# Performance work log

Hardware: AMD Instinct MI355X
Metric: run time of the kernel (lower is better)

Reference implementation:

```python
import jax, jax.numpy as jnp
import numpy as np

M, K, N, G = 64, 4096, 11008, 128  # tokens, infeatures, outfeatures, group_size
NUM_GROUPS = K // G  # 32


def _fp8_round_trip(w):
    # Simulate FP8 E4M3 storage of the quantized weight codes.
    return w.astype(jnp.float8_e4m3fn).astype(jnp.float32)


def setup_inputs() -> dict:
    key = jax.random.key(0)
    k1, k2, k3, k4 = jax.random.split(key, 4)
    x = jax.random.normal(k1, (M, K), dtype=jnp.float32)
    # FP8-representable weight codes (post round-trip, stored as f32 values)
    weight = _fp8_round_trip(jax.random.normal(k2, (N, K), dtype=jnp.float32) * 2.0)
    # Per-(out_feature, group) dequant scales, strictly positive
    weight_scale = jax.random.uniform(k3, (N, NUM_GROUPS), dtype=jnp.float32,
                                      minval=0.005, maxval=0.02)
    bias = jax.random.normal(k4, (N,), dtype=jnp.float32)
    return {"x": x, "weight": weight, "weight_scale": weight_scale, "bias": bias}


def reference(x, weight, weight_scale, bias):
    # Dequantize: each group of `G` consecutive in-features of an output row
    # shares one scale -> w_deq[o, i] = weight[o, i] * scale[o, i // G]
    n, k = weight.shape
    g = k // weight_scale.shape[1]
    w_deq = (weight.reshape(n, -1, g) * weight_scale[:, :, None]).reshape(n, k)
    # Fused dequant-matmul: out[m, o] = sum_i x[m, i] * w_deq[o, i] + bias[o]
    out = jnp.einsum("mk,nk->mn", x, w_deq) + bias
    return out
```

## Files before the change

kernel.cpp:

```cpp
#include <hip/hip_runtime.h>


#define Md 64
#define Kd 4096
#define Nd 11008
#define NGROUPS 32
#define BN 64
#define BK 64
#define KSPLIT 8
#define KCHUNK (Kd / KSPLIT)
#define NITER (KCHUNK / BK)
#define NGRP (KCHUNK / 128)
#define XLD (BK + 8)

typedef __attribute__((ext_vector_type(8))) __bf16 bf16x8;
typedef __attribute__((ext_vector_type(4))) float f32x4;

__global__ __launch_bounds__(256, 4)
void qlinear_pass1(const float* __restrict__ x,
                   const float* __restrict__ w,
                   const float* __restrict__ scale,
                   float* __restrict__ ws)
{
    const int tid  = threadIdx.x;
    const int wv   = tid >> 6;
    const int lane = tid & 63;
    const int quad = lane >> 4;
    const int ln   = lane & 15;

    const int n0 = blockIdx.x * BN;
    const int ky = blockIdx.y;
    const int k0 = ky * KCHUNK;

    const int nrow = n0 + wv * 16 + ln;
    const float* wp = w + (size_t)nrow * Kd + k0 + quad * 8;

    const int xrow = tid >> 2;
    const int xc0  = (tid & 3) * 16;
    const float* xp = x + (size_t)xrow * Kd + k0 + xc0;

    __shared__ __bf16 lds_x[Md * XLD];

    float4 sc4 = *(const float4*)(scale + (size_t)nrow * NGROUPS + ky * NGRP);
    const float sc[4] = {sc4.x, sc4.y, sc4.z, sc4.w};

    f32x4 acc[4];
    #pragma unroll
    for (int t = 0; t < 4; ++t) acc[t] = (f32x4){0.f, 0.f, 0.f, 0.f};

    float4 wreg[2][4], xreg[2][4];
    #pragma unroll
    for (int j = 0; j < 4; ++j)
        xreg[0][j] = *(const float4*)(xp + j * 4);
    wreg[0][0] = *(const float4*)(wp + 0);
    wreg[0][1] = *(const float4*)(wp + 4);
    wreg[0][2] = *(const float4*)(wp + 32);
    wreg[0][3] = *(const float4*)(wp + 36);

    #pragma unroll
    for (int g = 0; g < NGRP; ++g) {
        f32x4 pg[4];
        #pragma unroll
        for (int t = 0; t < 4; ++t) pg[t] = (f32x4){0.f, 0.f, 0.f, 0.f};

        #pragma unroll
        for (int sub = 0; sub < 2; ++sub) {
            const int i   = g * 2 + sub;
            const int buf = i & 1;

            #pragma unroll
            for (int j = 0; j < 2; ++j) {
                float4 a = xreg[buf][2 * j], b = xreg[buf][2 * j + 1];
                bf16x8 v = {(__bf16)a.x, (__bf16)a.y, (__bf16)a.z, (__bf16)a.w,
                            (__bf16)b.x, (__bf16)b.y, (__bf16)b.z, (__bf16)b.w};
                *(bf16x8*)&lds_x[xrow * XLD + xc0 + j * 8] = v;
            }
            __syncthreads();

            if (i + 1 < NITER) {
                const int nb = buf ^ 1;
                #pragma unroll
                for (int j = 0; j < 4; ++j)
                    xreg[nb][j] = *(const float4*)(xp + (i + 1) * BK + j * 4);
                wreg[nb][0] = *(const float4*)(wp + (i + 1) * BK + 0);
                wreg[nb][1] = *(const float4*)(wp + (i + 1) * BK + 4);
                wreg[nb][2] = *(const float4*)(wp + (i + 1) * BK + 32);
                wreg[nb][3] = *(const float4*)(wp + (i + 1) * BK + 36);
            }

            #pragma unroll
            for (int ks = 0; ks < 2; ++ks) {
                float4 wa = wreg[buf][2 * ks], wb = wreg[buf][2 * ks + 1];
                bf16x8 wf = {(__bf16)wa.x, (__bf16)wa.y, (__bf16)wa.z, (__bf16)wa.w,
                             (__bf16)wb.x, (__bf16)wb.y, (__bf16)wb.z, (__bf16)wb.w};
                #pragma unroll
                for (int t = 0; t < 4; ++t) {
                    bf16x8 xf = *(const bf16x8*)
                        &lds_x[(t * 16 + ln) * XLD + ks * 32 + quad * 8];
                    pg[t] = __builtin_amdgcn_mfma_f32_16x16x32_bf16(xf, wf, pg[t],
                                                                    0, 0, 0);
                }
            }
            __syncthreads();
        }

        const float s = sc[g];
        #pragma unroll
        for (int t = 0; t < 4; ++t)
            #pragma unroll
            for (int r = 0; r < 4; ++r)
                acc[t][r] += s * pg[t][r];
    }

    float* op = ws + ((size_t)ky * Md) * Nd + n0 + wv * 16 + ln;
    #pragma unroll
    for (int t = 0; t < 4; ++t)
        #pragma unroll
        for (int r = 0; r < 4; ++r)
            op[(size_t)(t * 16 + quad * 4 + r) * Nd] = acc[t][r];
}

__global__ __launch_bounds__(256)
void qlinear_reduce(const float* __restrict__ ws,
                    const float* __restrict__ bias,
                    float* __restrict__ out)
{
    const int idx = blockIdx.x * 256 + threadIdx.x;
    if (idx >= Md * Nd) return;
    const int n = idx % Nd;
    float v = bias[n];
    #pragma unroll
    for (int ky = 0; ky < KSPLIT; ++ky)
        v += ws[(size_t)ky * Md * Nd + idx];
    out[idx] = v;
}

extern "C" void kernel_launch(void* const* d_in, const int* in_sizes, int n_in,
                              void* d_out, int out_size, void* d_ws, size_t ws_size,
                              hipStream_t stream) {
    const float* x     = (const float*)d_in[0];
    const float* w     = (const float*)d_in[1];
    const float* scale = (const float*)d_in[2];
    const float* bias  = (const float*)d_in[3];
    float* out = (float*)d_out;
    float* ws  = (float*)d_ws;

    dim3 grid1(Nd / BN, KSPLIT);
    qlinear_pass1<<<grid1, 256, 0, stream>>>(x, w, scale, ws);

    const int total = Md * Nd;
    qlinear_reduce<<<(total + 255) / 256, 256, 0, stream>>>(ws, bias, out);
}
```

Baseline: 275.4 us.

## Pre-convert activations to MFMA-fragment bf16 layout and drop LDS staging

Adds an xprep kernel that converts x to bf16 once, laid out in MFMA fragment order. The main kernel can then load activation fragments straight from global memory (L2-resident) instead of each block converting x, staging it in LDS and synchronising twice per iteration. It also removes the explicit register double-buffering of weight loads and vectorises the split-K reduce to float4. The trade-offs are an extra kernel launch and reliance on the compiler and cache to hide load latency without the manual prefetch.

After: 279.6 us. About the same (+1.5%).

```diff
diff --git a/kernel.cpp b/kernel.cpp
--- a/kernel.cpp
+++ b/kernel.cpp
@@ -6,19 +6,34 @@
 #define Nd 11008
 #define NGROUPS 32
 #define BN 64
-#define BK 64
 #define KSPLIT 8
 #define KCHUNK (Kd / KSPLIT)
-#define NITER (KCHUNK / BK)
 #define NGRP (KCHUNK / 128)
-#define XLD (BK + 8)
+#define KBC (KCHUNK / 32)
 
 typedef __attribute__((ext_vector_type(8))) __bf16 bf16x8;
 typedef __attribute__((ext_vector_type(4))) float f32x4;
 
+
+__global__ __launch_bounds__(256)
+void xprep(const float* __restrict__ x, __bf16* __restrict__ xf)
+{
+    const int tid  = blockIdx.x * 256 + threadIdx.x;
+    const int lane = tid & 63;
+    const int t    = (tid >> 6) & 3;
+    const int kb   = tid >> 8;
+    const int row  = t * 16 + (lane & 15);
+    const int col  = kb * 32 + (lane >> 4) * 8;
+    const float4 a = *(const float4*)(x + (size_t)row * Kd + col);
+    const float4 b = *(const float4*)(x + (size_t)row * Kd + col + 4);
+    bf16x8 v = {(__bf16)a.x, (__bf16)a.y, (__bf16)a.z, (__bf16)a.w,
+                (__bf16)b.x, (__bf16)b.y, (__bf16)b.z, (__bf16)b.w};
+    *(bf16x8*)(xf + (size_t)tid * 8) = v;
+}
+
 __global__ __launch_bounds__(256, 4)
-void qlinear_pass1(const float* __restrict__ x,
-                   const float* __restrict__ w,
+void qlinear_pass1(const float* __restrict__ w,
+                   const __bf16* __restrict__ xf,
                    const float* __restrict__ scale,
                    float* __restrict__ ws)
 {
@@ -35,11 +50,7 @@
     const int nrow = n0 + wv * 16 + ln;
     const float* wp = w + (size_t)nrow * Kd + k0 + quad * 8;
 
-    const int xrow = tid >> 2;
-    const int xc0  = (tid & 3) * 16;
-    const float* xp = x + (size_t)xrow * Kd + k0 + xc0;
-
-    __shared__ __bf16 lds_x[Md * XLD];
+    const __bf16* xp = xf + (size_t)ky * KBC * 4 * 512 + lane * 8;
 
     float4 sc4 = *(const float4*)(scale + (size_t)nrow * NGROUPS + ky * NGRP);
     const float sc[4] = {sc4.x, sc4.y, sc4.z, sc4.w};
@@ -48,15 +59,6 @@
     #pragma unroll
     for (int t = 0; t < 4; ++t) acc[t] = (f32x4){0.f, 0.f, 0.f, 0.f};
 
-    float4 wreg[2][4], xreg[2][4];
-    #pragma unroll
-    for (int j = 0; j < 4; ++j)
-        xreg[0][j] = *(const float4*)(xp + j * 4);
-    wreg[0][0] = *(const float4*)(wp + 0);
-    wreg[0][1] = *(const float4*)(wp + 4);
-    wreg[0][2] = *(const float4*)(wp + 32);
-    wreg[0][3] = *(const float4*)(wp + 36);
-
     #pragma unroll
     for (int g = 0; g < NGRP; ++g) {
         f32x4 pg[4];
@@ -64,44 +66,18 @@
         for (int t = 0; t < 4; ++t) pg[t] = (f32x4){0.f, 0.f, 0.f, 0.f};
 
         #pragma unroll
-        for (int sub = 0; sub < 2; ++sub) {
-            const int i   = g * 2 + sub;
-            const int buf = i & 1;
-
+        for (int s = 0; s < 4; ++s) {
+            const int kb = g * 4 + s;
+            float4 wa = *(const float4*)(wp + kb * 32);
+            float4 wb = *(const float4*)(wp + kb * 32 + 4);
+            bf16x8 wf = {(__bf16)wa.x, (__bf16)wa.y, (__bf16)wa.z, (__bf16)wa.w,
+                         (__bf16)wb.x, (__bf16)wb.y, (__bf16)wb.z, (__bf16)wb.w};
             #pragma unroll
-            for (int j = 0; j < 2; ++j) {
-                float4 a = xreg[buf][2 * j], b = xreg[buf][2 * j + 1];
-                bf16x8 v = {(__bf16)a.x, (__bf16)a.y, (__bf16)a.z, (__bf16)a.w,
-                            (__bf16)b.x, (__bf16)b.y, (__bf16)b.z, (__bf16)b.w};
-                *(bf16x8*)&lds_x[xrow * XLD + xc0 + j * 8] = v;
+            for (int t = 0; t < 4; ++t) {
+                bf16x8 xv = *(const bf16x8*)(xp + ((size_t)kb * 4 + t) * 512);
+                pg[t] = __builtin_amdgcn_mfma_f32_16x16x32_bf16(xv, wf, pg[t],
+                                                                0, 0, 0);
             }
-            __syncthreads();
-
-            if (i + 1 < NITER) {
-                const int nb = buf ^ 1;
-                #pragma unroll
-                for (int j = 0; j < 4; ++j)
-                    xreg[nb][j] = *(const float4*)(xp + (i + 1) * BK + j * 4);
-                wreg[nb][0] = *(const float4*)(wp + (i + 1) * BK + 0);
-                wreg[nb][1] = *(const float4*)(wp + (i + 1) * BK + 4);
-                wreg[nb][2] = *(const float4*)(wp + (i + 1) * BK + 32);
-                wreg[nb][3] = *(const float4*)(wp + (i + 1) * BK + 36);
-            }
-
-            #pragma unroll
-            for (int ks = 0; ks < 2; ++ks) {
-                float4 wa = wreg[buf][2 * ks], wb = wreg[buf][2 * ks + 1];
-                bf16x8 wf = {(__bf16)wa.x, (__bf16)wa.y, (__bf16)wa.z, (__bf16)wa.w,
-                             (__bf16)wb.x, (__bf16)wb.y, (__bf16)wb.z, (__bf16)wb.w};
-                #pragma unroll
-                for (int t = 0; t < 4; ++t) {
-                    bf16x8 xf = *(const bf16x8*)
-                        &lds_x[(t * 16 + ln) * XLD + ks * 32 + quad * 8];
-                    pg[t] = __builtin_amdgcn_mfma_f32_16x16x32_bf16(xf, wf, pg[t],
-                                                                    0, 0, 0);
-                }
-            }
-            __syncthreads();
         }
 
         const float s = sc[g];
@@ -125,14 +101,16 @@
                     const float* __restrict__ bias,
                     float* __restrict__ out)
 {
-    const int idx = blockIdx.x * 256 + threadIdx.x;
-    if (idx >= Md * Nd) return;
-    const int n = idx % Nd;
-    float v = bias[n];
+    const int i4 = blockIdx.x * 256 + threadIdx.x;
+    if (i4 >= (Md * Nd) / 4) return;
+    const int n = (i4 * 4) % Nd;
+    float4 v = *(const float4*)(bias + n);
     #pragma unroll
-    for (int ky = 0; ky < KSPLIT; ++ky)
-        v += ws[(size_t)ky * Md * Nd + idx];
-    out[idx] = v;
+    for (int ky = 0; ky < KSPLIT; ++ky) {
+        float4 p = *(const float4*)(ws + (size_t)ky * Md * Nd + (size_t)i4 * 4);
+        v.x += p.x; v.y += p.y; v.z += p.z; v.w += p.w;
+    }
+    *(float4*)(out + (size_t)i4 * 4) = v;
 }
 
 extern "C" void kernel_launch(void* const* d_in, const int* in_sizes, int n_in,
@@ -145,9 +123,12 @@
     float* out = (float*)d_out;
     float* ws  = (float*)d_ws;
 
+    __bf16* xf = (__bf16*)(ws + (size_t)KSPLIT * Md * Nd);
+
+    xprep<<<128, 256, 0, stream>>>(x, xf);
+
     dim3 grid1(Nd / BN, KSPLIT);
-    qlinear_pass1<<<grid1, 256, 0, stream>>>(x, w, scale, ws);
+    qlinear_pass1<<<grid1, 256, 0, stream>>>(w, xf, scale, ws);
 
-    const int total = Md * Nd;
-    qlinear_reduce<<<(total + 255) / 256, 256, 0, stream>>>(ws, bias, out);
+    qlinear_reduce<<<(Md * Nd / 4 + 255) / 256, 256, 0, stream>>>(ws, bias, out);
 }
```
